# Kernel tuning notes

Measured on AMD Instinct MI355X. Metric: run time of the kernel, lower is better.

## Reference

```python
import jax, jax.numpy as jnp
import numpy as np

EPS = 1e-8
TEMPERATURE = 0.5


def setup_inputs() -> dict:
    key = jax.random.key(0)
    k1, k2, k3, k4 = jax.random.split(key, 4)
    B, DIN, DOUT = 4096, 2048, 128
    return {
        "zi": jax.random.normal(k1, (B, DIN), dtype=jnp.float32),
        "zj": jax.random.normal(k2, (B, DIN), dtype=jnp.float32),
        "W": jax.random.normal(k3, (DOUT, DIN), dtype=jnp.float32) * 0.02,
        "b": jax.random.normal(k4, (DOUT,), dtype=jnp.float32) * 0.02,
    }


def reference(zi, zj, W, b):
    # MLP projection head: Linear(ReLU(x))
    hi = jax.nn.relu(zi) @ W.T + b  # [B, 128]
    hj = jax.nn.relu(zj) @ W.T + b  # [B, 128]
    B = hi.shape[0]
    N = 2 * B
    reps = jnp.concatenate([hi, hj], axis=0)  # [2B, 128]
    # Cosine similarity: normalize once (torch eps=1e-8 clamp), then one matmul
    norms = jnp.maximum(jnp.linalg.norm(reps, axis=-1, keepdims=True), EPS)
    zn = reps / norms
    sim = (zn @ zn.T) / TEMPERATURE  # [2B, 2B]
    idx = jnp.arange(N)
    # positive pair index: i <-> i +/- B
    pos = sim[idx, (idx + B) % N]  # [2B]
    # denominator: all j != i (self excluded, positive included once) ==
    # torch's [positive, negatives(mask excludes diag and +/-B diags)] logits
    NEG_INF = jnp.asarray(-1e9, sim.dtype)
    sim_masked = jnp.where(idx[:, None] == idx[None, :], NEG_INF, sim)
    lse = jax.scipy.special.logsumexp(sim_masked, axis=1)  # [2B]
    loss = jnp.mean(lse - pos)
    return loss
```

## Files before the change

kernel.cpp:

```cpp
#include <hip/hip_runtime.h>
#include <math.h>

#define DIN    2048
#define DOUT   128
#define BHALF  4096
#define NTOT   8192
#define NSPLIT 8
#define JSPAN  1024

typedef __bf16 bf16x8 __attribute__((ext_vector_type(8)));
typedef float  f32x4  __attribute__((ext_vector_type(4)));
typedef unsigned int u32x4 __attribute__((ext_vector_type(4)));

#define MFMA16 __builtin_amdgcn_mfma_f32_16x16x32_bf16

struct PackedPair { unsigned int h, l; };

__device__ __forceinline__ unsigned int bf16_rne(float f) {
    unsigned int u = __float_as_uint(f);
    return (u + 0x7fffu + ((u >> 16) & 1u)) >> 16;
}
__device__ __forceinline__ float bf16f(unsigned int h) {
    return __uint_as_float(h << 16);
}
__device__ __forceinline__ PackedPair split2(float a, float b) {
    unsigned int h0 = bf16_rne(a), h1 = bf16_rne(b);
    unsigned int g0 = bf16_rne(a - bf16f(h0)), g1 = bf16_rne(b - bf16f(h1));
    PackedPair r;
    r.h = h0 | (h1 << 16);
    r.l = g0 | (g1 << 16);
    return r;
}


__global__ __launch_bounds__(256) void wsplit_kernel(
    const float* __restrict__ W,
    unsigned short* __restrict__ Whp, unsigned short* __restrict__ Wlp,
    float* __restrict__ out)
{
    int t = blockIdx.x * 256 + threadIdx.x;
    if (t == 0) out[0] = 0.f;
    int l  = t & 63;
    int ks = (t >> 6) & 63;
    int g  = t >> 12;
    int c  = g * 16 + (l & 15);
    int k0 = ks * 32 + ((l >> 4) << 3);
    const float* src = W + (size_t)c * DIN + k0;
    f32x4 v0 = *(const f32x4*)src;
    f32x4 v1 = *(const f32x4*)(src + 4);
    u32x4 hv, lv;
    PackedPair p0 = split2(v0[0], v0[1]);  hv[0] = p0.h; lv[0] = p0.l;
    PackedPair p1 = split2(v0[2], v0[3]);  hv[1] = p1.h; lv[1] = p1.l;
    PackedPair p2 = split2(v1[0], v1[1]);  hv[2] = p2.h; lv[2] = p2.l;
    PackedPair p3 = split2(v1[2], v1[3]);  hv[3] = p3.h; lv[3] = p3.l;
    size_t off = ((size_t)(g * 64 + ks) * 64 + l) * 8;
    *(u32x4*)(Whp + off) = hv;
    *(u32x4*)(Wlp + off) = lv;
}

__global__ __launch_bounds__(512, 4) void proj_kernel(
    const float* __restrict__ zi, const float* __restrict__ zj,
    const unsigned short* __restrict__ Whp, const unsigned short* __restrict__ Wlp,
    const float* __restrict__ bvec,
    unsigned short* __restrict__ Zhp, unsigned short* __restrict__ Zlp)
{
    __shared__ float Red[4][16][132];
    const int t = threadIdx.x;
    const int w = t >> 6;
    const int lane = t & 63;
    const int r15 = lane & 15, q = lane >> 4;
    const int row0 = blockIdx.x * 16;
    const float* zsrc = (row0 < BHALF) ? zi : zj;
    const int zr0 = (row0 < BHALF) ? row0 : row0 - BHALF;

    f32x4 acc[8];
    #pragma unroll
    for (int g = 0; g < 8; g++) acc[g] = (f32x4){0.f, 0.f, 0.f, 0.f};

    const float* zrow = zsrc + (size_t)(zr0 + r15) * DIN + q * 8;
    f32x4 pv0 = *(const f32x4*)(zrow + w * 256);
    f32x4 pv1 = *(const f32x4*)(zrow + w * 256 + 4);

    #pragma unroll
    for (int i = 0; i < 8; i++) {
        const int ks = w * 8 + i;
        f32x4 v0 = pv0, v1 = pv1;
        if (i < 7) {
            pv0 = *(const f32x4*)(zrow + w * 256 + (i + 1) * 32);
            pv1 = *(const f32x4*)(zrow + w * 256 + (i + 1) * 32 + 4);
        }
        #pragma unroll
        for (int p = 0; p < 4; p++) {
            v0[p] = fmaxf(v0[p], 0.f);
            v1[p] = fmaxf(v1[p], 0.f);
        }
        u32x4 hv, lv;
        PackedPair p0 = split2(v0[0], v0[1]);  hv[0] = p0.h; lv[0] = p0.l;
        PackedPair p1 = split2(v0[2], v0[3]);  hv[1] = p1.h; lv[1] = p1.l;
        PackedPair p2 = split2(v1[0], v1[1]);  hv[2] = p2.h; lv[2] = p2.l;
        PackedPair p3 = split2(v1[2], v1[3]);  hv[3] = p3.h; lv[3] = p3.l;
        bf16x8 ah = __builtin_bit_cast(bf16x8, hv);
        bf16x8 al = __builtin_bit_cast(bf16x8, lv);
        #pragma unroll
        for (int g = 0; g < 8; g++) {
            size_t bo = ((size_t)(g * 64 + ks) * 64 + lane) * 8;
            bf16x8 bh = __builtin_bit_cast(bf16x8, *(const u32x4*)(Whp + bo));
            bf16x8 bl = __builtin_bit_cast(bf16x8, *(const u32x4*)(Wlp + bo));
            acc[g] = MFMA16(ah, bh, acc[g], 0, 0, 0);
            acc[g] = MFMA16(ah, bl, acc[g], 0, 0, 0);
            acc[g] = MFMA16(al, bh, acc[g], 0, 0, 0);
        }
    }

    if (w >= 4) {
        #pragma unroll
        for (int g = 0; g < 8; g++)
            #pragma unroll
            for (int r = 0; r < 4; r++)
                Red[w - 4][q * 4 + r][g * 16 + r15] = acc[g][r];
    }
    __syncthreads();
    if (w < 4) {
        #pragma unroll
        for (int g = 0; g < 8; g++)
            #pragma unroll
            for (int r = 0; r < 4; r++)
                Red[w][q * 4 + r][g * 16 + r15] += acc[g][r];
    }
    __syncthreads();

    const int row = t >> 5;
    const int tx  = t & 31;
    float v[4];
    #pragma unroll
    for (int j = 0; j < 4; j++) {
        v[j] = Red[0][row][tx * 4 + j] + Red[1][row][tx * 4 + j]
             + Red[2][row][tx * 4 + j] + Red[3][row][tx * 4 + j];
    }
    const f32x4 bb = *(const f32x4*)(bvec + tx * 4);
    v[0] += bb[0]; v[1] += bb[1]; v[2] += bb[2]; v[3] += bb[3];
    float ssq = v[0]*v[0] + v[1]*v[1] + v[2]*v[2] + v[3]*v[3];
    #pragma unroll
    for (int msk = 1; msk < 32; msk <<= 1) ssq += __shfl_xor(ssq, msk);
    const float inv = 1.f / fmaxf(sqrtf(ssq), 1e-8f);
    const int grow = row0 + row;
    const int gg = grow >> 4, rr = grow & 15;
    #pragma unroll
    for (int j = 0; j < 4; j++) {
        const int k = tx * 4 + j;
        float x = v[j] * inv;
        unsigned int h  = bf16_rne(x);
        unsigned int lo = bf16_rne(x - bf16f(h));
        size_t off = (((size_t)gg * 4 + (k >> 5)) * 64
                      + (rr | (((k >> 3) & 3) << 4))) * 8 + (k & 7);
        Zhp[off] = (unsigned short)h;
        Zlp[off] = (unsigned short)lo;
    }
}

__global__ __launch_bounds__(256, 2) void sim_kernel(
    const unsigned short* __restrict__ Zhp, const unsigned short* __restrict__ Zlp,
    float* __restrict__ Spart, float* __restrict__ P)
{
    __shared__ unsigned short Jt[2][16384];
    const int t = threadIdx.x;
    const int w = t >> 6, lane = t & 63;
    const int r15 = lane & 15, rq = lane >> 4;
    const int jsplit = blockIdx.x & 7;
    const int iblk   = blockIdx.x >> 3;
    const int rowbase = iblk * 128 + w * 32;
    const int j0base  = jsplit * JSPAN;

#define STAGE(jt_, buf_) do {                                                 \
        const int jref_ = (j0base >> 4) + (jt_) * 4;                          \
        _Pragma("unroll")                                                     \
        for (int rr_ = 0; rr_ < 8; rr_++) {                                   \
            const int cid_ = rr_ * 4 + w;                                     \
            const int hl_ = cid_ >> 4, jg_ = (cid_ >> 2) & 3, ks_ = cid_ & 3; \
            const unsigned short* src_ = hl_ ? Zlp : Zhp;                     \
            const unsigned short* gp_ = src_ +                                \
                (((size_t)(jref_ + jg_) * 4 + ks_) * 64 + lane) * 8;          \
            unsigned short* lp_ = &Jt[buf_][(cid_ * 64) * 8];                 \
            __builtin_amdgcn_global_load_lds(                                 \
                (const __attribute__((address_space(1))) unsigned int*)gp_,   \
                (__attribute__((address_space(3))) unsigned int*)lp_,         \
                16, 0, 0);                                                    \
        } } while (0)

    STAGE(0, 0);

    bf16x8 Ah[2][4], Al[2][4];
    #pragma unroll
    for (int m = 0; m < 2; m++) {
        const int gA = iblk * 8 + w * 2 + m;
        #pragma unroll
        for (int ks = 0; ks < 4; ks++) {
            size_t ao = (((size_t)gA * 4 + ks) * 64 + lane) * 8;
            Ah[m][ks] = __builtin_bit_cast(bf16x8, *(const u32x4*)(Zhp + ao));
            Al[m][ks] = __builtin_bit_cast(bf16x8, *(const u32x4*)(Zlp + ao));
        }
    }

    float rs[2][4], ps[2][4];
    #pragma unroll
    for (int m = 0; m < 2; m++)
        #pragma unroll
        for (int r = 0; r < 4; r++) { rs[m][r] = 0.f; ps[m][r] = 0.f; }

    #pragma unroll 2
    for (int jt = 0; jt < 16; jt++) {
        const int cur = jt & 1;
        const int j0 = j0base + jt * 64;
        if (jt < 15) {
            STAGE(jt + 1, cur ^ 1);
            asm volatile("s_waitcnt vmcnt(8)" ::: "memory");
        } else {
            asm volatile("s_waitcnt vmcnt(0)" ::: "memory");
        }
        __builtin_amdgcn_s_barrier();
        __builtin_amdgcn_sched_barrier(0);

        const unsigned short* J = &Jt[cur][0];
        f32x4 acc[2][4];
        #pragma unroll
        for (int m = 0; m < 2; m++)
            #pragma unroll
            for (int jg = 0; jg < 4; jg++) acc[m][jg] = (f32x4){0.f,0.f,0.f,0.f};

        #pragma unroll
        for (int ks = 0; ks < 4; ks++) {
            #pragma unroll
            for (int jg = 0; jg < 4; jg++) {
                bf16x8 bh = __builtin_bit_cast(bf16x8,
                    *(const u32x4*)&J[((jg * 4 + ks) * 64 + lane) * 8]);
                bf16x8 bl = __builtin_bit_cast(bf16x8,
                    *(const u32x4*)&J[((jg * 4 + ks + 16) * 64 + lane) * 8]);
                #pragma unroll
                for (int m = 0; m < 2; m++) {
                    acc[m][jg] = MFMA16(Ah[m][ks], bh, acc[m][jg], 0, 0, 0);
                    acc[m][jg] = MFMA16(Ah[m][ks], bl, acc[m][jg], 0, 0, 0);
                    acc[m][jg] = MFMA16(Al[m][ks], bh, acc[m][jg], 0, 0, 0);
                }
            }
        }

        #pragma unroll
        for (int m = 0; m < 2; m++) {
            const int rb16 = rowbase + m * 16;
            #pragma unroll
            for (int jg = 0; jg < 4; jg++) {
                const int cb16 = j0 + jg * 16;
                if (cb16 != rb16 && cb16 != (rb16 ^ BHALF)) {
                    #pragma unroll
                    for (int r = 0; r < 4; r++)
                        rs[m][r] += __expf(2.f * acc[m][jg][r]);
                } else {
                    const int gcol = cb16 + r15;
                    #pragma unroll
                    for (int r = 0; r < 4; r++) {
                        float s = 2.f * acc[m][jg][r];
                        const int grow = rb16 + rq * 4 + r;
                        float e = __expf(s);
                        if (gcol == grow) e = 0.f;
                        rs[m][r] += e;
                        if (gcol == (grow ^ BHALF)) ps[m][r] += s;
                    }
                }
            }
        }
        __builtin_amdgcn_sched_barrier(0);
        __builtin_amdgcn_s_barrier();
    }
#undef STAGE

    #pragma unroll
    for (int m = 0; m < 2; m++)
        #pragma unroll
        for (int r = 0; r < 4; r++) {
            float a = rs[m][r], p = ps[m][r];
            #pragma unroll
            for (int msk = 1; msk < 16; msk <<= 1) {
                a += __shfl_xor(a, msk);
                p += __shfl_xor(p, msk);
            }
            if (r15 == 0) {
                const int grow = rowbase + m * 16 + rq * 4 + r;
                Spart[jsplit * NTOT + grow] = a;
                if (((grow ^ BHALF) >> 10) == jsplit) P[grow] = p;
            }
        }
}

__global__ __launch_bounds__(256) void loss_kernel(
    const float* __restrict__ Spart, const float* __restrict__ P,
    float* __restrict__ out)
{
    const int i = blockIdx.x * 256 + threadIdx.x;
    float ssum = 0.f;
    #pragma unroll
    for (int sp = 0; sp < NSPLIT; sp++) ssum += Spart[sp * NTOT + i];
    float v = logf(ssum) - P[i];
    #pragma unroll
    for (int msk = 1; msk < 64; msk <<= 1) v += __shfl_xor(v, msk);
    __shared__ float red[4];
    if ((threadIdx.x & 63) == 0) red[threadIdx.x >> 6] = v;
    __syncthreads();
    if (threadIdx.x == 0)
        atomicAdd(out, (red[0] + red[1] + red[2] + red[3]) * (1.f / (float)NTOT));
}

extern "C" void kernel_launch(void* const* d_in, const int* in_sizes, int n_in,
                              void* d_out, int out_size, void* d_ws, size_t ws_size,
                              hipStream_t stream) {
    const float* zi = (const float*)d_in[0];
    const float* zj = (const float*)d_in[1];
    const float* W  = (const float*)d_in[2];
    const float* bv = (const float*)d_in[3];
    float* out = (float*)d_out;

    char* ws = (char*)d_ws;
    unsigned short* Whp = (unsigned short*)(ws);
    unsigned short* Wlp = (unsigned short*)(ws + (512 << 10));
    unsigned short* Zhp = (unsigned short*)(ws + (1024 << 10));
    unsigned short* Zlp = (unsigned short*)(ws + (3072 << 10));
    float* Spart = (float*)(ws);
    float* P     = (float*)(ws + (256 << 10));

    wsplit_kernel<<<128, 256, 0, stream>>>(W, Whp, Wlp, out);
    proj_kernel<<<512, 512, 0, stream>>>(zi, zj, Whp, Wlp, bv, Zhp, Zlp);
    sim_kernel<<<512, 256, 0, stream>>>(Zhp, Zlp, Spart, P);
    loss_kernel<<<NTOT / 256, 256, 0, stream>>>(Spart, P, out);
}
```

Measured before the change: 171.2 us.

## Split projection GEMM over K with partial-sum reduction; enlarge sim tiles

Adds a K-split projection kernel in which each block computes a 64-row by 128-column tile over a quarter of DIN. Each W fragment loaded is reused across four row groups, and the partial results go to a workspace buffer. A separate reduce kernel then adds bias, normalises, and packs the bf16 hi/lo operands. The similarity kernel moves to 512 threads covering 256 rows with 16 column splits of 512 and a smaller staging depth. The new path only runs if the workspace is at least 21 MB and costs extra global traffic plus one more launch; otherwise the old projection kernel is used.

```diff
diff --git a/kernel.cpp b/kernel.cpp
--- a/kernel.cpp
+++ b/kernel.cpp
@@ -5,8 +5,8 @@
 #define DOUT   128
 #define BHALF  4096
 #define NTOT   8192
-#define NSPLIT 8
-#define JSPAN  1024
+#define NSPLIT 16
+#define JSPAN  512
 
 typedef __bf16 bf16x8 __attribute__((ext_vector_type(8)));
 typedef float  f32x4  __attribute__((ext_vector_type(4)));
@@ -58,93 +58,106 @@
     *(u32x4*)(Wlp + off) = lv;
 }
 
-__global__ __launch_bounds__(512, 4) void proj_kernel(
+__global__ __launch_bounds__(512, 4) void projp_kernel(
     const float* __restrict__ zi, const float* __restrict__ zj,
     const unsigned short* __restrict__ Whp, const unsigned short* __restrict__ Wlp,
-    const float* __restrict__ bvec,
-    unsigned short* __restrict__ Zhp, unsigned short* __restrict__ Zlp)
-{
-    __shared__ float Red[4][16][132];
+    float* __restrict__ Hpart)
+{
+    __shared__ float Red[4][2][16][68];
     const int t = threadIdx.x;
-    const int w = t >> 6;
-    const int lane = t & 63;
+    const int w = t >> 6, lane = t & 63;
     const int r15 = lane & 15, q = lane >> 4;
-    const int row0 = blockIdx.x * 16;
+    const int kq = w & 3, gh = w >> 2;
+    const int rg = blockIdx.x >> 2;
+    const int kp = blockIdx.x & 3;
+    const int row0 = rg * 64;
     const float* zsrc = (row0 < BHALF) ? zi : zj;
     const int zr0 = (row0 < BHALF) ? row0 : row0 - BHALF;
 
-    f32x4 acc[8];
-    #pragma unroll
-    for (int g = 0; g < 8; g++) acc[g] = (f32x4){0.f, 0.f, 0.f, 0.f};
-
-    const float* zrow = zsrc + (size_t)(zr0 + r15) * DIN + q * 8;
-    f32x4 pv0 = *(const f32x4*)(zrow + w * 256);
-    f32x4 pv1 = *(const f32x4*)(zrow + w * 256 + 4);
-
-    #pragma unroll
-    for (int i = 0; i < 8; i++) {
-        const int ks = w * 8 + i;
-        f32x4 v0 = pv0, v1 = pv1;
-        if (i < 7) {
-            pv0 = *(const f32x4*)(zrow + w * 256 + (i + 1) * 32);
-            pv1 = *(const f32x4*)(zrow + w * 256 + (i + 1) * 32 + 4);
-        }
-        #pragma unroll
-        for (int p = 0; p < 4; p++) {
-            v0[p] = fmaxf(v0[p], 0.f);
-            v1[p] = fmaxf(v1[p], 0.f);
-        }
-        u32x4 hv, lv;
-        PackedPair p0 = split2(v0[0], v0[1]);  hv[0] = p0.h; lv[0] = p0.l;
-        PackedPair p1 = split2(v0[2], v0[3]);  hv[1] = p1.h; lv[1] = p1.l;
-        PackedPair p2 = split2(v1[0], v1[1]);  hv[2] = p2.h; lv[2] = p2.l;
-        PackedPair p3 = split2(v1[2], v1[3]);  hv[3] = p3.h; lv[3] = p3.l;
-        bf16x8 ah = __builtin_bit_cast(bf16x8, hv);
-        bf16x8 al = __builtin_bit_cast(bf16x8, lv);
-        #pragma unroll
-        for (int g = 0; g < 8; g++) {
+    f32x4 acc[4][4];
+    #pragma unroll
+    for (int m = 0; m < 4; m++)
+        #pragma unroll
+        for (int jg = 0; jg < 4; jg++) acc[m][jg] = (f32x4){0.f,0.f,0.f,0.f};
+
+    const int kbase = kp * 512 + kq * 128;
+    const float* zlane = zsrc + (size_t)(zr0 + r15) * DIN + kbase + q * 8;
+
+    #pragma unroll
+    for (int i = 0; i < 4; i++) {
+        const int ks = (kbase >> 5) + i;
+        bf16x8 bh[4], bl[4];
+        #pragma unroll
+        for (int jg = 0; jg < 4; jg++) {
+            const int g = gh * 4 + jg;
             size_t bo = ((size_t)(g * 64 + ks) * 64 + lane) * 8;
-            bf16x8 bh = __builtin_bit_cast(bf16x8, *(const u32x4*)(Whp + bo));
-            bf16x8 bl = __builtin_bit_cast(bf16x8, *(const u32x4*)(Wlp + bo));
-            acc[g] = MFMA16(ah, bh, acc[g], 0, 0, 0);
-            acc[g] = MFMA16(ah, bl, acc[g], 0, 0, 0);
-            acc[g] = MFMA16(al, bh, acc[g], 0, 0, 0);
-        }
-    }
-
-    if (w >= 4) {
-        #pragma unroll
-        for (int g = 0; g < 8; g++)
+            bh[jg] = __builtin_bit_cast(bf16x8, *(const u32x4*)(Whp + bo));
+            bl[jg] = __builtin_bit_cast(bf16x8, *(const u32x4*)(Wlp + bo));
+        }
+        #pragma unroll
+        for (int m = 0; m < 4; m++) {
+            const float* s = zlane + (size_t)(m * 16) * DIN + i * 32;
+            f32x4 v0 = *(const f32x4*)s;
+            f32x4 v1 = *(const f32x4*)(s + 4);
+            #pragma unroll
+            for (int p = 0; p < 4; p++) {
+                v0[p] = fmaxf(v0[p], 0.f);
+                v1[p] = fmaxf(v1[p], 0.f);
+            }
+            u32x4 hv, lv;
+            PackedPair p0 = split2(v0[0], v0[1]);  hv[0] = p0.h; lv[0] = p0.l;
+            PackedPair p1 = split2(v0[2], v0[3]);  hv[1] = p1.h; lv[1] = p1.l;
+            PackedPair p2 = split2(v1[0], v1[1]);  hv[2] = p2.h; lv[2] = p2.l;
+            PackedPair p3 = split2(v1[2], v1[3]);  hv[3] = p3.h; lv[3] = p3.l;
+            bf16x8 ah = __builtin_bit_cast(bf16x8, hv);
+            bf16x8 al = __builtin_bit_cast(bf16x8, lv);
+            #pragma unroll
+            for (int jg = 0; jg < 4; jg++) {
+                acc[m][jg] = MFMA16(ah, bh[jg], acc[m][jg], 0, 0, 0);
+                acc[m][jg] = MFMA16(ah, bl[jg], acc[m][jg], 0, 0, 0);
+                acc[m][jg] = MFMA16(al, bh[jg], acc[m][jg], 0, 0, 0);
+            }
+        }
+    }
+
+    #pragma unroll
+    for (int m = 0; m < 4; m++) {
+        __syncthreads();
+        #pragma unroll
+        for (int jg = 0; jg < 4; jg++)
             #pragma unroll
             for (int r = 0; r < 4; r++)
-                Red[w - 4][q * 4 + r][g * 16 + r15] = acc[g][r];
-    }
-    __syncthreads();
-    if (w < 4) {
-        #pragma unroll
-        for (int g = 0; g < 8; g++)
-            #pragma unroll
-            for (int r = 0; r < 4; r++)
-                Red[w][q * 4 + r][g * 16 + r15] += acc[g][r];
-    }
-    __syncthreads();
-
-    const int row = t >> 5;
-    const int tx  = t & 31;
-    float v[4];
-    #pragma unroll
-    for (int j = 0; j < 4; j++) {
-        v[j] = Red[0][row][tx * 4 + j] + Red[1][row][tx * 4 + j]
-             + Red[2][row][tx * 4 + j] + Red[3][row][tx * 4 + j];
-    }
-    const f32x4 bb = *(const f32x4*)(bvec + tx * 4);
-    v[0] += bb[0]; v[1] += bb[1]; v[2] += bb[2]; v[3] += bb[3];
+                Red[kq][gh][q * 4 + r][jg * 16 + r15] = acc[m][jg][r];
+        __syncthreads();
+        {
+            const int gh2 = t >> 8, rem = t & 255;
+            const int row = rem >> 4, c4 = rem & 15;
+            f32x4 s = *(const f32x4*)&Red[0][gh2][row][c4 * 4];
+            s += *(const f32x4*)&Red[1][gh2][row][c4 * 4];
+            s += *(const f32x4*)&Red[2][gh2][row][c4 * 4];
+            s += *(const f32x4*)&Red[3][gh2][row][c4 * 4];
+            *(f32x4*)&Hpart[((size_t)kp * NTOT + row0 + m * 16 + row) * DOUT
+                            + gh2 * 64 + c4 * 4] = s;
+        }
+    }
+}
+
+__global__ __launch_bounds__(256) void hreduce_kernel(
+    const float* __restrict__ Hpart, const float* __restrict__ bvec,
+    unsigned short* __restrict__ Zhp, unsigned short* __restrict__ Zlp)
+{
+    const int i = blockIdx.x * 256 + threadIdx.x;
+    const int row = i >> 5, tx = i & 31;
+    f32x4 v = (f32x4){0.f, 0.f, 0.f, 0.f};
+    #pragma unroll
+    for (int kp = 0; kp < 4; kp++)
+        v += *(const f32x4*)&Hpart[((size_t)kp * NTOT + row) * DOUT + tx * 4];
+    v += *(const f32x4*)(bvec + tx * 4);
     float ssq = v[0]*v[0] + v[1]*v[1] + v[2]*v[2] + v[3]*v[3];
     #pragma unroll
     for (int msk = 1; msk < 32; msk <<= 1) ssq += __shfl_xor(ssq, msk);
     const float inv = 1.f / fmaxf(sqrtf(ssq), 1e-8f);
-    const int grow = row0 + row;
-    const int gg = grow >> 4, rr = grow & 15;
+    const int gg = row >> 4, rr = row & 15;
     #pragma unroll
     for (int j = 0; j < 4; j++) {
         const int k = tx * 4 + j;
@@ -158,7 +171,107 @@
     }
 }
 
-__global__ __launch_bounds__(256, 2) void sim_kernel(
+__global__ __launch_bounds__(512, 4) void proj_kernel(
+    const float* __restrict__ zi, const float* __restrict__ zj,
+    const unsigned short* __restrict__ Whp, const unsigned short* __restrict__ Wlp,
+    const float* __restrict__ bvec,
+    unsigned short* __restrict__ Zhp, unsigned short* __restrict__ Zlp)
+{
+    __shared__ float Red[4][16][132];
+    const int t = threadIdx.x;
+    const int w = t >> 6;
+    const int lane = t & 63;
+    const int r15 = lane & 15, q = lane >> 4;
+    const int row0 = blockIdx.x * 16;
+    const float* zsrc = (row0 < BHALF) ? zi : zj;
+    const int zr0 = (row0 < BHALF) ? row0 : row0 - BHALF;
+
+    f32x4 acc[8];
+    #pragma unroll
+    for (int g = 0; g < 8; g++) acc[g] = (f32x4){0.f, 0.f, 0.f, 0.f};
+
+    const float* zrow = zsrc + (size_t)(zr0 + r15) * DIN + q * 8;
+    f32x4 pv0 = *(const f32x4*)(zrow + w * 256);
+    f32x4 pv1 = *(const f32x4*)(zrow + w * 256 + 4);
+
+    #pragma unroll
+    for (int i = 0; i < 8; i++) {
+        const int ks = w * 8 + i;
+        f32x4 v0 = pv0, v1 = pv1;
+        if (i < 7) {
+            pv0 = *(const f32x4*)(zrow + w * 256 + (i + 1) * 32);
+            pv1 = *(const f32x4*)(zrow + w * 256 + (i + 1) * 32 + 4);
+        }
+        #pragma unroll
+        for (int p = 0; p < 4; p++) {
+            v0[p] = fmaxf(v0[p], 0.f);
+            v1[p] = fmaxf(v1[p], 0.f);
+        }
+        u32x4 hv, lv;
+        PackedPair p0 = split2(v0[0], v0[1]);  hv[0] = p0.h; lv[0] = p0.l;
+        PackedPair p1 = split2(v0[2], v0[3]);  hv[1] = p1.h; lv[1] = p1.l;
+        PackedPair p2 = split2(v1[0], v1[1]);  hv[2] = p2.h; lv[2] = p2.l;
+        PackedPair p3 = split2(v1[2], v1[3]);  hv[3] = p3.h; lv[3] = p3.l;
+        bf16x8 ah = __builtin_bit_cast(bf16x8, hv);
+        bf16x8 al = __builtin_bit_cast(bf16x8, lv);
+        #pragma unroll
+        for (int g = 0; g < 8; g++) {
+            size_t bo = ((size_t)(g * 64 + ks) * 64 + lane) * 8;
+            bf16x8 bh = __builtin_bit_cast(bf16x8, *(const u32x4*)(Whp + bo));
+            bf16x8 bl = __builtin_bit_cast(bf16x8, *(const u32x4*)(Wlp + bo));
+            acc[g] = MFMA16(ah, bh, acc[g], 0, 0, 0);
+            acc[g] = MFMA16(ah, bl, acc[g], 0, 0, 0);
+            acc[g] = MFMA16(al, bh, acc[g], 0, 0, 0);
+        }
+    }
+
+    if (w >= 4) {
+        #pragma unroll
+        for (int g = 0; g < 8; g++)
+            #pragma unroll
+            for (int r = 0; r < 4; r++)
+                Red[w - 4][q * 4 + r][g * 16 + r15] = acc[g][r];
+    }
+    __syncthreads();
+    if (w < 4) {
+        #pragma unroll
+        for (int g = 0; g < 8; g++)
+            #pragma unroll
+            for (int r = 0; r < 4; r++)
+                Red[w][q * 4 + r][g * 16 + r15] += acc[g][r];
+    }
+    __syncthreads();
+
+    const int row = t >> 5;
+    const int tx  = t & 31;
+    float v[4];
+    #pragma unroll
+    for (int j = 0; j < 4; j++) {
+        v[j] = Red[0][row][tx * 4 + j] + Red[1][row][tx * 4 + j]
+             + Red[2][row][tx * 4 + j] + Red[3][row][tx * 4 + j];
+    }
+    const f32x4 bb = *(const f32x4*)(bvec + tx * 4);
+    v[0] += bb[0]; v[1] += bb[1]; v[2] += bb[2]; v[3] += bb[3];
+    float ssq = v[0]*v[0] + v[1]*v[1] + v[2]*v[2] + v[3]*v[3];
+    #pragma unroll
+    for (int msk = 1; msk < 32; msk <<= 1) ssq += __shfl_xor(ssq, msk);
+    const float inv = 1.f / fmaxf(sqrtf(ssq), 1e-8f);
+    const int grow = row0 + row;
+    const int gg = grow >> 4, rr = grow & 15;
+    #pragma unroll
+    for (int j = 0; j < 4; j++) {
+        const int k = tx * 4 + j;
+        float x = v[j] * inv;
+        unsigned int h  = bf16_rne(x);
+        unsigned int lo = bf16_rne(x - bf16f(h));
+        size_t off = (((size_t)gg * 4 + (k >> 5)) * 64
+                      + (rr | (((k >> 3) & 3) << 4))) * 8 + (k & 7);
+        Zhp[off] = (unsigned short)h;
+        Zlp[off] = (unsigned short)lo;
+    }
+}
+
+__global__ __launch_bounds__(512, 4) void sim_kernel(
     const unsigned short* __restrict__ Zhp, const unsigned short* __restrict__ Zlp,
     float* __restrict__ Spart, float* __restrict__ P)
 {
@@ -166,16 +279,16 @@
     const int t = threadIdx.x;
     const int w = t >> 6, lane = t & 63;
     const int r15 = lane & 15, rq = lane >> 4;
-    const int jsplit = blockIdx.x & 7;
-    const int iblk   = blockIdx.x >> 3;
-    const int rowbase = iblk * 128 + w * 32;
+    const int jsplit = ((blockIdx.x & 7) << 1) | ((blockIdx.x >> 3) & 1);
+    const int iblk   = blockIdx.x >> 4;
+    const int rowbase = iblk * 256 + w * 32;
     const int j0base  = jsplit * JSPAN;
 
 #define STAGE(jt_, buf_) do {                                                 \
         const int jref_ = (j0base >> 4) + (jt_) * 4;                          \
         _Pragma("unroll")                                                     \
-        for (int rr_ = 0; rr_ < 8; rr_++) {                                   \
-            const int cid_ = rr_ * 4 + w;                                     \
+        for (int rr_ = 0; rr_ < 4; rr_++) {                                   \
+            const int cid_ = rr_ * 8 + w;                                     \
             const int hl_ = cid_ >> 4, jg_ = (cid_ >> 2) & 3, ks_ = cid_ & 3; \
             const unsigned short* src_ = hl_ ? Zlp : Zhp;                     \
             const unsigned short* gp_ = src_ +                                \
@@ -192,7 +305,7 @@
     bf16x8 Ah[2][4], Al[2][4];
     #pragma unroll
     for (int m = 0; m < 2; m++) {
-        const int gA = iblk * 8 + w * 2 + m;
+        const int gA = iblk * 16 + w * 2 + m;
         #pragma unroll
         for (int ks = 0; ks < 4; ks++) {
             size_t ao = (((size_t)gA * 4 + ks) * 64 + lane) * 8;
@@ -208,12 +321,12 @@
         for (int r = 0; r < 4; r++) { rs[m][r] = 0.f; ps[m][r] = 0.f; }
 
     #pragma unroll 2
-    for (int jt = 0; jt < 16; jt++) {
+    for (int jt = 0; jt < JSPAN / 64; jt++) {
         const int cur = jt & 1;
         const int j0 = j0base + jt * 64;
-        if (jt < 15) {
+        if (jt < JSPAN / 64 - 1) {
             STAGE(jt + 1, cur ^ 1);
-            asm volatile("s_waitcnt vmcnt(8)" ::: "memory");
+            asm volatile("s_waitcnt vmcnt(4)" ::: "memory");
         } else {
             asm volatile("s_waitcnt vmcnt(0)" ::: "memory");
         }
@@ -286,7 +399,7 @@
             if (r15 == 0) {
                 const int grow = rowbase + m * 16 + rq * 4 + r;
                 Spart[jsplit * NTOT + grow] = a;
-                if (((grow ^ BHALF) >> 10) == jsplit) P[grow] = p;
+                if (((grow ^ BHALF) >> 9) == jsplit) P[grow] = p;
             }
         }
 }
@@ -323,11 +436,17 @@
     unsigned short* Wlp = (unsigned short*)(ws + (512 << 10));
     unsigned short* Zhp = (unsigned short*)(ws + (1024 << 10));
     unsigned short* Zlp = (unsigned short*)(ws + (3072 << 10));
+    float* Hpart = (float*)(ws + (5120 << 10));
     float* Spart = (float*)(ws);
-    float* P     = (float*)(ws + (256 << 10));
+    float* P     = (float*)(ws + (512 << 10));
 
     wsplit_kernel<<<128, 256, 0, stream>>>(W, Whp, Wlp, out);
-    proj_kernel<<<512, 512, 0, stream>>>(zi, zj, Whp, Wlp, bv, Zhp, Zlp);
-    sim_kernel<<<512, 256, 0, stream>>>(Zhp, Zlp, Spart, P);
+    if (ws_size >= (size_t)(21u << 20)) {
+        projp_kernel<<<512, 512, 0, stream>>>(zi, zj, Whp, Wlp, Hpart);
+        hreduce_kernel<<<1024, 256, 0, stream>>>(Hpart, bv, Zhp, Zlp);
+    } else {
+        proj_kernel<<<512, 512, 0, stream>>>(zi, zj, Whp, Wlp, bv, Zhp, Zlp);
+    }
+    sim_kernel<<<512, 512, 0, stream>>>(Zhp, Zlp, Spart, P);
     loss_kernel<<<NTOT / 256, 256, 0, stream>>>(Spart, P, out);
 }
```

New measurement: 258.4 us. +50.9%, slower.
